# Optimization experiments

Hardware: AMD Instinct MI355X
Metric: run time of the kernel (lower is better)

The kernel has to match this reference:

```python
import jax, jax.numpy as jnp
import numpy as np

T, B, U = 64, 2048, 1024


def setup_inputs() -> dict:
    key = jax.random.key(0)
    ks = jax.random.split(key, 7)
    inputs = jax.random.normal(ks[0], (T, B, 1), dtype=jnp.float32)
    x1_0 = jax.random.normal(ks[1], (B, 1), dtype=jnp.float32)
    x2_0 = jax.random.normal(ks[2], (B, 1), dtype=jnp.float32)
    c0 = jax.random.normal(ks[3], (B, U), dtype=jnp.float32)
    kernel = jax.random.normal(ks[4], (1, 2 * U), dtype=jnp.float32) * 0.05
    # orthogonal-ish recurrent kernel, scaled for stability
    recurrent_kernel = jax.random.normal(ks[5], (U, 2 * U), dtype=jnp.float32) * (1.0 / np.sqrt(U))
    # unit_forget_bias: ones for the f gate, zeros for the c gate
    bias = jnp.concatenate([jnp.ones((U,), jnp.float32), jnp.zeros((U,), jnp.float32)])
    output_kernel = jax.random.normal(ks[6], (U, 1), dtype=jnp.float32) * 0.05
    return {"inputs": inputs, "x1_0": x1_0, "x2_0": x2_0, "c0": c0,
            "kernel": kernel, "recurrent_kernel": recurrent_kernel,
            "bias": bias, "output_kernel": output_kernel}


def reference(inputs, x1_0, x2_0, c0, kernel, recurrent_kernel, bias, output_kernel):
    U = c0.shape[-1]
    Kf, Kc = kernel[:, :U], kernel[:, U:2 * U]          # [1,U] each
    Rf, Rc = recurrent_kernel[:, :U], recurrent_kernel[:, U:2 * U]  # [U,U]
    bf, bc = bias[:U], bias[U:2 * U]

    def step(carry, inp):
        x1, x2, h = carry                 # x1,x2: [B,1]; h (= c_{t-1}): [B,U]
        x_f = h @ Rf + x1 @ Kf + bf       # [B,U]
        x_c = h @ Rc + x1 @ Kc + bc       # [B,U]
        f = jax.nn.sigmoid(x_f)
        c = f * h + (1.0 - f) * jnp.tanh(x_c)
        x1_new = x1 + x2                  # double-integrator position update
        x2_new = x2 + inp * (c @ output_kernel)  # velocity driven by scalar input * readout
        return (x1_new, x2_new, c), x1_new

    _, outputs = jax.lax.scan(step, (x1_0, x2_0, c0), inputs)
    return outputs  # [T, B, 1]
```

## Files before the change

kernel.cpp:

```cpp
#include <hip/hip_runtime.h>
#include <hip/hip_bf16.h>

#define T_STEPS 64
#define B_DIM 2048
#define U_DIM 1024

#define BM 128
#define BU 64
#define BK 32
#define KITERS (U_DIM / BK)
#define NST 3
#define STG 8192

typedef __attribute__((ext_vector_type(8))) _Float16 h8;
typedef __attribute__((ext_vector_type(4))) float f4;

__device__ __forceinline__ void async_cp16(const _Float16* g, _Float16* l) {
    __builtin_amdgcn_global_load_lds((const __attribute__((address_space(1))) void*)g,
                                     (__attribute__((address_space(3))) void*)l,
                                     16, 0, 0);
}


__global__ void transpose_R(const float* __restrict__ R, _Float16* __restrict__ Rt) {
    __shared__ float tile[32][33];
    int nb = blockIdx.x * 32;
    int kb = blockIdx.y * 32;
    int tx = threadIdx.x, ty = threadIdx.y;
    #pragma unroll
    for (int i = ty; i < 32; i += 8)
        tile[i][tx] = R[(size_t)(kb + i) * (2 * U_DIM) + nb + tx];
    __syncthreads();
    #pragma unroll
    for (int i = ty; i < 32; i += 8)
        Rt[(size_t)(nb + i) * U_DIM + kb + tx] = (_Float16)tile[tx][i];
}

__global__ void init_state(const float* __restrict__ c0, _Float16* __restrict__ h0,
                           float* __restrict__ y) {
    int i = blockIdx.x * 256 + threadIdx.x;
    h0[i] = (_Float16)c0[i];
    if (i < 3 * B_DIM) y[i] = 0.f;
}

__global__ __launch_bounds__(256, 2) void gemm_step(
    const _Float16* __restrict__ hA, _Float16* __restrict__ hB,
    const _Float16* __restrict__ Rt,
    const float* __restrict__ x1_0, const float* __restrict__ x2_0,
    float* __restrict__ x1w,
    float* __restrict__ x2w,
    const float* __restrict__ kern, const float* __restrict__ bias,
    const float* __restrict__ okern,
    float* __restrict__ y,
    const float* __restrict__ inputs,
    float* __restrict__ out,
    int t)
{
    __shared__ __align__(16) _Float16 lS[NST][STG];
    __shared__ float x1s[BM];

    const int tid    = threadIdx.x;
    const int wid    = tid >> 6;
    const int lane   = tid & 63;
    const int lane15 = lane & 15;
    const int quad   = lane >> 4;
    const int u0     = blockIdx.x * BU;
    const int b0     = blockIdx.y * BM;
    const int wrow   = (wid >> 1) * 64;
    const int wcol   = (wid & 1) * 32;

    if (tid < BM) {
        const int b = b0 + tid;
        float x1n, x2n;
        if (t == 0) {
            x1n = x1_0[b];
            x2n = x2_0[b];
        } else {
            const int rd = (t + 1) & 1;
            const float x1p = x1w[rd * B_DIM + b];
            const float x2p = x2w[rd * B_DIM + b];
            const float yp  = y[((t + 2) % 3) * B_DIM + b];
            const float ip  = inputs[(size_t)(t - 1) * B_DIM + b];
            x1n = x1p + x2p;
            x2n = x2p + ip * yp;
        }
        x1s[tid] = x1n;
        if (blockIdx.x == 0) {
            const int wr = t & 1;
            x1w[wr * B_DIM + b] = x1n;
            x2w[wr * B_DIM + b] = x2n;
            if (t > 0) out[(size_t)(t - 1) * B_DIM + b] = x1n;
            y[((t + 1) % 3) * B_DIM + b] = 0.f;
        }
    }

    float kf[2], kc[2], bf_[2], bc_[2], ok_[2];
    #pragma unroll
    for (int nt = 0; nt < 2; ++nt) {
        const int u = u0 + wcol + nt * 16 + lane15;
        kf[nt] = kern[u];
        kc[nt] = kern[U_DIM + u];
        bf_[nt] = bias[u];
        bc_[nt] = bias[U_DIM + u];
        ok_[nt] = okern[u];
    }
    _Float16 hv[4][2][4];
    #pragma unroll
    for (int mt = 0; mt < 4; ++mt)
        #pragma unroll
        for (int nt = 0; nt < 2; ++nt)
            #pragma unroll
            for (int reg = 0; reg < 4; ++reg)
                hv[mt][nt][reg] = hA[(size_t)(b0 + wrow + mt * 16 + quad * 4 + reg) * U_DIM
                                     + u0 + wcol + nt * 16 + lane15];

    const int srow  = lane >> 2;
    const int schnk = ((lane & 3) ^ (srow & 3)) * 8;
    auto stage = [&](int buf, int kt) {
        const int k0 = kt * BK;
        #pragma unroll
        for (int j = 0; j < 2; ++j) {
            const int r = wid * 2 + j;
            async_cp16(hA + (size_t)(b0 + r * 16 + srow) * U_DIM + k0 + schnk,
                       &lS[buf][r * 512]);
        }
        async_cp16(Rt + (size_t)(u0 + wid * 16 + srow) * U_DIM + k0 + schnk,
                   &lS[buf][4096 + wid * 512]);
        async_cp16(Rt + (size_t)(U_DIM + u0 + wid * 16 + srow) * U_DIM + k0 + schnk,
                   &lS[buf][6144 + wid * 512]);
    };
    stage(0, 0);
    stage(1, 1);

    f4 accF[4][2], accC[4][2];
    #pragma unroll
    for (int mt = 0; mt < 4; ++mt)
        #pragma unroll
        for (int nt = 0; nt < 2; ++nt) {
            accF[mt][nt] = (f4){0.f, 0.f, 0.f, 0.f};
            accC[mt][nt] = (f4){0.f, 0.f, 0.f, 0.f};
        }

    for (int kt = 0; kt < KITERS; ++kt) {
        const int cur = kt % 3;
        if (kt < KITERS - 1)
            __builtin_amdgcn_s_waitcnt(0x0F74);
        else
            __builtin_amdgcn_s_waitcnt(0x0F70);
        __syncthreads();
        if (kt + 2 < KITERS) stage((kt + 2) % 3, kt + 2);

        h8 af[4], bff[2], bfc[2];
        #pragma unroll
        for (int mt = 0; mt < 4; ++mt) {
            const int R = wrow + mt * 16 + lane15;
            af[mt] = *(const h8*)&lS[cur][(R >> 4) * 512 + lane15 * 32 +
                                          ((quad ^ (lane15 & 3)) * 8)];
        }
        #pragma unroll
        for (int nt = 0; nt < 2; ++nt) {
            const int Rb = wcol + nt * 16 + lane15;
            const int off = (Rb >> 4) * 512 + lane15 * 32 + ((quad ^ (lane15 & 3)) * 8);
            bff[nt] = *(const h8*)&lS[cur][4096 + off];
            bfc[nt] = *(const h8*)&lS[cur][6144 + off];
        }
        #pragma unroll
        for (int mt = 0; mt < 4; ++mt)
            #pragma unroll
            for (int nt = 0; nt < 2; ++nt) {
                accF[mt][nt] = __builtin_amdgcn_mfma_f32_16x16x32_f16(af[mt], bff[nt], accF[mt][nt], 0, 0, 0);
                accC[mt][nt] = __builtin_amdgcn_mfma_f32_16x16x32_f16(af[mt], bfc[nt], accC[mt][nt], 0, 0, 0);
            }
    }

    __syncthreads();

    _Float16* lC = &lS[0][0];
    float* ycur = y + (t % 3) * B_DIM;
    #pragma unroll
    for (int mt = 0; mt < 4; ++mt) {
        const int rlb = wrow + mt * 16 + quad * 4;
        float psum[4] = {0.f, 0.f, 0.f, 0.f};
        #pragma unroll
        for (int nt = 0; nt < 2; ++nt) {
            const int ul = wcol + nt * 16 + lane15;
            #pragma unroll
            for (int reg = 0; reg < 4; ++reg) {
                const int rl = rlb + reg;
                const float x1 = x1s[rl];
                const float xf = accF[mt][nt][reg] + x1 * kf[nt] + bf_[nt];
                const float xc = accC[mt][nt][reg] + x1 * kc[nt] + bc_[nt];
                const float fg = 1.f / (1.f + __expf(-xf));
                const float th = 1.f - 2.f / (1.f + __expf(2.f * xc));
                const float cv = fg * (float)hv[mt][nt][reg] + (1.f - fg) * th;
                lC[rl * 72 + ul] = (_Float16)cv;
                psum[reg] += cv * ok_[nt];
            }
        }
        #pragma unroll
        for (int reg = 0; reg < 4; ++reg) {
            float s = psum[reg];
            s += __shfl_xor(s, 1);
            s += __shfl_xor(s, 2);
            s += __shfl_xor(s, 4);
            s += __shfl_xor(s, 8);
            if (lane15 == 0) atomicAdd(&ycur[b0 + rlb + reg], s);
        }
    }

    __syncthreads();
    #pragma unroll
    for (int j = 0; j < 4; ++j) {
        const int idx = j * 256 + tid;
        const int row = idx >> 3;
        const int col = idx & 7;
        *(uint4*)&hB[(size_t)(b0 + row) * U_DIM + u0 + col * 8] =
            *(const uint4*)&lC[row * 72 + col * 8];
    }
}

__global__ void finish(const float* __restrict__ x1w1, const float* __restrict__ x2w1,
                       float* __restrict__ out_last) {
    const int i = blockIdx.x * 256 + threadIdx.x;
    out_last[i] = x1w1[i] + x2w1[i];
}

extern "C" void kernel_launch(void* const* d_in, const int* in_sizes, int n_in,
                              void* d_out, int out_size, void* d_ws, size_t ws_size,
                              hipStream_t stream) {
    const float* inputs = (const float*)d_in[0];
    const float* x1_0   = (const float*)d_in[1];
    const float* x2_0   = (const float*)d_in[2];
    const float* c0     = (const float*)d_in[3];
    const float* kern   = (const float*)d_in[4];
    const float* rker   = (const float*)d_in[5];
    const float* bias   = (const float*)d_in[6];
    const float* okern  = (const float*)d_in[7];
    float* out = (float*)d_out;

    _Float16* Rt = (_Float16*)d_ws;
    _Float16* h0 = Rt + (size_t)2 * U_DIM * U_DIM;
    _Float16* h1 = h0 + (size_t)B_DIM * U_DIM;
    float* y   = (float*)(h1 + (size_t)B_DIM * U_DIM);
    float* x1w = y + 3 * B_DIM;
    float* x2w = x1w + 2 * B_DIM;

    transpose_R<<<dim3(64, 32), dim3(32, 8), 0, stream>>>(rker, Rt);
    init_state<<<dim3(B_DIM * U_DIM / 256), dim3(256), 0, stream>>>(c0, h0, y);

    _Float16* hcur = h0;
    _Float16* hnxt = h1;
    for (int t = 0; t < T_STEPS; ++t) {
        gemm_step<<<dim3(U_DIM / BU, B_DIM / BM), dim3(256), 0, stream>>>(
            hcur, hnxt, Rt, x1_0, x2_0, x1w, x2w, kern, bias, okern, y,
            inputs, out, t);
        _Float16* tmp = hcur; hcur = hnxt; hnxt = tmp;
    }
    finish<<<dim3(B_DIM / 256), dim3(256), 0, stream>>>(
        x1w + B_DIM, x2w + B_DIM, out + (size_t)(T_STEPS - 1) * B_DIM);
}
```

Before: 1.536 ms.

## Give each wave private LDS tiles and drop per-iteration block barriers

Each wave now stages its own A rows and R columns into a private LDS region, so the K loop needs only a vmcnt wait per step instead of a block-wide __syncthreads. The pipeline also goes from three to four stages. The aim is to stop waves stalling on each other at every K step. In exchange, waves that share rows or columns now load the same data separately, which doubles global/L2 traffic for LDS fills. LDS use grows, and launch bounds drop to one block per CU.

```diff
diff --git a/kernel.cpp b/kernel.cpp
--- a/kernel.cpp
+++ b/kernel.cpp
@@ -9,8 +9,7 @@
 #define BU 64
 #define BK 32
 #define KITERS (U_DIM / BK)
-#define NST 3
-#define STG 8192
+#define NSTG 4
 
 typedef __attribute__((ext_vector_type(8))) _Float16 h8;
 typedef __attribute__((ext_vector_type(4))) float f4;
@@ -43,7 +42,7 @@
     if (i < 3 * B_DIM) y[i] = 0.f;
 }
 
-__global__ __launch_bounds__(256, 2) void gemm_step(
+__global__ __launch_bounds__(256, 1) void gemm_step(
     const _Float16* __restrict__ hA, _Float16* __restrict__ hB,
     const _Float16* __restrict__ Rt,
     const float* __restrict__ x1_0, const float* __restrict__ x2_0,
@@ -56,7 +55,7 @@
     float* __restrict__ out,
     int t)
 {
-    __shared__ __align__(16) _Float16 lS[NST][STG];
+    __shared__ __align__(16) _Float16 lS[4][NSTG][4096];
     __shared__ float x1s[BM];
 
     const int tid    = threadIdx.x;
@@ -116,21 +115,23 @@
 
     const int srow  = lane >> 2;
     const int schnk = ((lane & 3) ^ (srow & 3)) * 8;
-    auto stage = [&](int buf, int kt) {
+    auto stage = [&](int st, int kt) {
         const int k0 = kt * BK;
         #pragma unroll
+        for (int j = 0; j < 4; ++j)
+            async_cp16(hA + (size_t)(b0 + wrow + j * 16 + srow) * U_DIM + k0 + schnk,
+                       &lS[wid][st][j * 512]);
+        #pragma unroll
         for (int j = 0; j < 2; ++j) {
-            const int r = wid * 2 + j;
-            async_cp16(hA + (size_t)(b0 + r * 16 + srow) * U_DIM + k0 + schnk,
-                       &lS[buf][r * 512]);
-        }
-        async_cp16(Rt + (size_t)(u0 + wid * 16 + srow) * U_DIM + k0 + schnk,
-                   &lS[buf][4096 + wid * 512]);
-        async_cp16(Rt + (size_t)(U_DIM + u0 + wid * 16 + srow) * U_DIM + k0 + schnk,
-                   &lS[buf][6144 + wid * 512]);
+            async_cp16(Rt + (size_t)(u0 + wcol + j * 16 + srow) * U_DIM + k0 + schnk,
+                       &lS[wid][st][2048 + j * 512]);
+            async_cp16(Rt + (size_t)(U_DIM + u0 + wcol + j * 16 + srow) * U_DIM + k0 + schnk,
+                       &lS[wid][st][3072 + j * 512]);
+        }
     };
     stage(0, 0);
     stage(1, 1);
+    stage(2, 2);
 
     f4 accF[4][2], accC[4][2];
     #pragma unroll
@@ -141,28 +142,17 @@
             accC[mt][nt] = (f4){0.f, 0.f, 0.f, 0.f};
         }
 
-    for (int kt = 0; kt < KITERS; ++kt) {
-        const int cur = kt % 3;
-        if (kt < KITERS - 1)
-            __builtin_amdgcn_s_waitcnt(0x0F74);
-        else
-            __builtin_amdgcn_s_waitcnt(0x0F70);
-        __syncthreads();
-        if (kt + 2 < KITERS) stage((kt + 2) % 3, kt + 2);
-
+    const int sw = (quad ^ (lane15 & 3)) * 8;
+    auto body = [&](int kt) {
+        const int st = kt & 3;
         h8 af[4], bff[2], bfc[2];
         #pragma unroll
-        for (int mt = 0; mt < 4; ++mt) {
-            const int R = wrow + mt * 16 + lane15;
-            af[mt] = *(const h8*)&lS[cur][(R >> 4) * 512 + lane15 * 32 +
-                                          ((quad ^ (lane15 & 3)) * 8)];
-        }
+        for (int mt = 0; mt < 4; ++mt)
+            af[mt] = *(const h8*)&lS[wid][st][mt * 512 + lane15 * 32 + sw];
         #pragma unroll
         for (int nt = 0; nt < 2; ++nt) {
-            const int Rb = wcol + nt * 16 + lane15;
-            const int off = (Rb >> 4) * 512 + lane15 * 32 + ((quad ^ (lane15 & 3)) * 8);
-            bff[nt] = *(const h8*)&lS[cur][4096 + off];
-            bfc[nt] = *(const h8*)&lS[cur][6144 + off];
+            bff[nt] = *(const h8*)&lS[wid][st][2048 + nt * 512 + lane15 * 32 + sw];
+            bfc[nt] = *(const h8*)&lS[wid][st][3072 + nt * 512 + lane15 * 32 + sw];
         }
         #pragma unroll
         for (int mt = 0; mt < 4; ++mt)
@@ -171,11 +161,21 @@
                 accF[mt][nt] = __builtin_amdgcn_mfma_f32_16x16x32_f16(af[mt], bff[nt], accF[mt][nt], 0, 0, 0);
                 accC[mt][nt] = __builtin_amdgcn_mfma_f32_16x16x32_f16(af[mt], bfc[nt], accC[mt][nt], 0, 0, 0);
             }
-    }
+    };
+
+    for (int kt = 0; kt < KITERS - 2; ++kt) {
+        __builtin_amdgcn_s_waitcnt(0x4F70);
+        body(kt);
+        if (kt + 3 < KITERS) stage((kt + 3) & 3, kt + 3);
+    }
+    __builtin_amdgcn_s_waitcnt(0x0F78);
+    body(KITERS - 2);
+    __builtin_amdgcn_s_waitcnt(0x0F70);
+    body(KITERS - 1);
 
     __syncthreads();
 
-    _Float16* lC = &lS[0][0];
+    _Float16* lC = &lS[0][0][0];
     float* ycur = y + (t % 3) * B_DIM;
     #pragma unroll
     for (int mt = 0; mt < 4; ++mt) {
```

New measurement: 1.529 ms. No clear change (-0.4%).
